# Performance work log

Measured on AMD Instinct MI355X. Metric: run time of the kernel, lower is better.

## Reference

```python
import jax, jax.numpy as jnp
import numpy as np

V, EMB, HID, ENC = 32000, 512, 1024, 1024
B, T, TB = 64, 512, 512
PAD = 0


def setup_inputs() -> dict:
    key = jax.random.key(0)
    kk = jax.random.split(key, 24)
    w = lambda k, s: jax.random.normal(k, s, dtype=jnp.float32) * 0.02
    a = lambda k, s: jax.random.normal(k, s, dtype=jnp.float32)
    emb_table = w(kk[0], (V, EMB)).at[PAD].set(0.0)  # padding_idx row zeroed
    IN = EMB + ENC + HID  # lstm input size
    return {
        "y": jax.random.randint(kk[1], (B,), 0, V),
        "h": a(kk[2], (B, HID)),
        "c": a(kk[3], (B, HID)),
        "enc_out": a(kk[4], (B, T, ENC)),
        "bwd_states": a(kk[5], (B, TB, HID)),
        "src_ids": jax.random.randint(kk[6], (B, T), 0, V),
        "src_mask": jnp.ones((B, T), dtype=jnp.int32),
        "emb_table": emb_table,
        "W_ih": w(kk[7], (4 * HID, IN)),
        "W_hh": w(kk[8], (4 * HID, HID)),
        "b_ih": jnp.zeros((4 * HID,), jnp.float32),
        "b_hh": jnp.zeros((4 * HID,), jnp.float32),
        "Wq_e": w(kk[9], (HID, HID)),
        "Wk_e": w(kk[10], (HID, ENC)),
        "v_e": w(kk[11], (HID,)),
        "Wq_b": w(kk[12], (HID, HID)),
        "Wk_b": w(kk[13], (HID, HID)),
        "v_b": w(kk[14], (HID,)),
        "Wp": w(kk[15], (V, HID)),
        "bp": jnp.zeros((V,), jnp.float32),
        "wc": w(kk[16], (ENC,)),
        "ws": w(kk[17], (HID,)),
        "wy": w(kk[18], (EMB,)),
        "pg_b": jnp.zeros((), jnp.float32),
    }


def _bahdanau(query, keys, Wq, Wk, v, mask=None):
    # query [B,H], keys [B,T,D] -> context [B,D], attn [B,T]
    q = query @ Wq.T                                  # [B,A]
    k = jnp.einsum("btd,ad->bta", keys, Wk)           # [B,T,A]
    e = jnp.einsum("bta,a->bt", jnp.tanh(q[:, None, :] + k), v)
    if mask is not None:
        e = jnp.where(mask == 0, jnp.finfo(e.dtype).min, e)
    attn = jax.nn.softmax(e, axis=-1)
    ctx = jnp.einsum("bt,btd->bd", attn, keys)
    return ctx, attn


def reference(y, h, c, enc_out, bwd_states, src_ids, src_mask, emb_table,
              W_ih, W_hh, b_ih, b_hh, Wq_e, Wk_e, v_e, Wq_b, Wk_b, v_b,
              Wp, bp, wc, ws, wy, pg_b):
    emb = emb_table[y]                                # [B,EMB]
    query = h                                         # state[0].squeeze(0)
    c_enc, attn_enc = _bahdanau(query, enc_out, Wq_e, Wk_e, v_e, src_mask)
    c_bwd, _ = _bahdanau(query, bwd_states, Wq_b, Wk_b, v_b)
    x = jnp.concatenate([emb, c_enc, c_bwd], axis=-1)  # [B,EMB+ENC+HID]
    gates = x @ W_ih.T + h @ W_hh.T + b_ih + b_hh      # [B,4H], torch order i,f,g,o
    i, f, g, o = jnp.split(gates, 4, axis=-1)
    c_new = jax.nn.sigmoid(f) * c + jax.nn.sigmoid(i) * jnp.tanh(g)
    h_new = jax.nn.sigmoid(o) * jnp.tanh(c_new)
    vocab_dist = jax.nn.softmax(h_new @ Wp.T + bp, axis=-1)  # [B,V]
    p_gen = jax.nn.sigmoid(c_enc @ wc + h_new @ ws + emb @ wy + pg_b)[:, None]
    p_vocab = p_gen * vocab_dist
    copy_mask = (src_ids < V).astype(vocab_dist.dtype)
    safe_ids = jnp.minimum(src_ids, V - 1)
    contrib = (1.0 - p_gen) * attn_enc * copy_mask     # [B,T]
    scatter = jax.vmap(lambda idx, val: jnp.zeros((V,), val.dtype).at[idx].add(val))(safe_ids, contrib)
    final_dist = p_vocab + scatter
    return final_dist, h_new, c_new
```

## Files before the change

kernel.cpp:

```cpp
#include <hip/hip_runtime.h>
#include <hip/hip_bf16.h>

#define VSZ   32000
#define EMBD  512
#define HIDD  1024
#define BB    64
#define TSEQ  512
#define G4    4096

typedef short bf16x8 __attribute__((ext_vector_type(8)));
typedef float f32x4  __attribute__((ext_vector_type(4)));
typedef float f32x16 __attribute__((ext_vector_type(16)));

__device__ __forceinline__ float sigmoid_f(float x){ return 1.0f/(1.0f+__expf(-x)); }
__device__ __forceinline__ float fast_tanh(float x){
  float e = __expf(2.0f*x);
  return 1.0f - 2.0f*__builtin_amdgcn_rcpf(e + 1.0f);
}
__device__ __forceinline__ short f2bfs(float x){
  unsigned u = __float_as_uint(x);
  unsigned r = (u + 0x7FFFu + ((u>>16)&1u)) >> 16;
  return (short)r;
}
__device__ __forceinline__ bf16x8 cvt8(float4 a, float4 b){
  bf16x8 p;
  p[0]=f2bfs(a.x); p[1]=f2bfs(a.y); p[2]=f2bfs(a.z); p[3]=f2bfs(a.w);
  p[4]=f2bfs(b.x); p[5]=f2bfs(b.y); p[6]=f2bfs(b.z); p[7]=f2bfs(b.w);
  return p;
}
__device__ __forceinline__ float wave_sum(float x){
  #pragma unroll
  for (int off=32; off>0; off>>=1) x += __shfl_xor(x, off);
  return x;
}
__device__ __forceinline__ float wave_max(float x){
  #pragma unroll
  for (int off=32; off>0; off>>=1) x = fmaxf(x, __shfl_xor(x, off));
  return x;
}

__global__ __launch_bounds__(128) void k_embed(const int* __restrict__ y,
                                               const float* __restrict__ tab,
                                               float* __restrict__ emb){
  int b = blockIdx.x;
  int row = y[b];
  const float4* src = (const float4*)(tab + (size_t)row*EMBD);
  float4* dst = (float4*)(emb + (size_t)b*EMBD);
  dst[threadIdx.x] = src[threadIdx.x];
}

__global__ __launch_bounds__(256) void k_pack(const float* __restrict__ Wk,
                                              short* __restrict__ dst){
  int id = blockIdx.x*256 + threadIdx.x;
  int l = id & 63, s = (id>>6) & 63, nt = id >> 12;
  const float* src = Wk + (size_t)(nt*32 + (l&31))*1024 + s*16 + (l>>5)*8;
  float4 f0 = ((const float4*)src)[0], f1 = ((const float4*)src)[1];
  *(bf16x8*)(dst + (size_t)id*8) = cvt8(f0, f1);
}

__global__ __launch_bounds__(256) void k_prep_h(const float* __restrict__ h,
                                                short* __restrict__ xb){
  int id = blockIdx.x*256 + threadIdx.x;
  int b = id >> 7, d = (id & 127)*8;
  const float4* s = (const float4*)(h + (size_t)b*HIDD + d);
  *(bf16x8*)(xb + (size_t)b*3584 + 2560 + d) = cvt8(s[0], s[1]);
}

__global__ __launch_bounds__(256) void k_prep_x2(const float* __restrict__ emb,
                                                 const float* __restrict__ ctxe,
                                                 const float* __restrict__ ctxb,
                                                 short* __restrict__ xb){
  int id = blockIdx.x*256 + threadIdx.x;
  if (id >= 64*320) return;
  int b = id / 320, off = (id % 320)*8;
  const float* src;
  if (off < 512)        src = emb  + (size_t)b*EMBD + off;
  else if (off < 1536)  src = ctxe + (size_t)b*HIDD + (off-512);
  else                  src = ctxb + (size_t)b*HIDD + (off-1536);
  float4 f0 = ((const float4*)src)[0], f1 = ((const float4*)src)[1];
  *(bf16x8*)(xb + (size_t)b*3584 + off) = cvt8(f0, f1);
}

__global__ __launch_bounds__(256) void k_mm64(
    const short* __restrict__ A0, int lda0, const float* __restrict__ B0, int ldb0, int K0, float* __restrict__ out0, int ldo0,
    const short* __restrict__ A1, int lda1, const float* __restrict__ B1, int ldb1, int K1, float* __restrict__ out1, int ldo1){
  const short* A; const float* B; float* out; int lda, ldb, K, ldo;
  if (blockIdx.z == 0){ A=A0; B=B0; out=out0; lda=lda0; ldb=ldb0; K=K0; ldo=ldo0; }
  else                { A=A1; B=B1; out=out1; lda=lda1; ldb=ldb1; K=K1; ldo=ldo1; }
  int tid = threadIdx.x, l = tid & 63, w = tid >> 6;
  int l15 = l & 15, l4 = l >> 4;
  int n0 = blockIdx.x*256 + w*64;
  int kper = K / gridDim.y;
  int dbeg = blockIdx.y * kper, dend = dbeg + kper;
  f32x4 acc[4][4];
  #pragma unroll
  for (int i=0;i<4;i++)
    #pragma unroll
    for (int j=0;j<4;j++)
      #pragma unroll
      for (int r=0;r<4;r++) acc[i][j][r]=0.f;
  for (int d0=dbeg; d0<dend; d0+=32){
    bf16x8 af[4];
    #pragma unroll
    for (int ms=0; ms<4; ms++)
      af[ms] = *(const bf16x8*)(A + (size_t)(ms*16 + l15)*lda + d0 + l4*8);
    bf16x8 bfr[4];
    #pragma unroll
    for (int ni=0; ni<4; ni++){
      const float* bp = B + (size_t)(n0 + ni*16 + l15)*ldb + d0 + l4*8;
      float4 f0 = ((const float4*)bp)[0], f1 = ((const float4*)bp)[1];
      bfr[ni] = cvt8(f0, f1);
    }
    #pragma unroll
    for (int ms=0; ms<4; ms++)
      #pragma unroll
      for (int ni=0; ni<4; ni++)
        acc[ms][ni] = __builtin_amdgcn_mfma_f32_16x16x32_bf16(af[ms], bfr[ni], acc[ms][ni], 0,0,0);
  }
  float* op = out + (size_t)blockIdx.y * 64 * ldo;
  #pragma unroll
  for (int ms=0; ms<4; ms++)
    #pragma unroll
    for (int ni=0; ni<4; ni++)
      #pragma unroll
      for (int r=0; r<4; r++){
        int m = ms*16 + l4*4 + r;
        op[(size_t)m*ldo + n0 + ni*16 + l15] = acc[ms][ni][r];
      }
}

__global__ __launch_bounds__(256) void k_qred(const float* __restrict__ qpe,
                                              const float* __restrict__ qpb,
                                              float* __restrict__ qe,
                                              float* __restrict__ qb){
  int id = blockIdx.x*256 + threadIdx.x;
  int sel = id >> 16, i = id & 65535;
  const float* p = (sel ? qpb : qpe) + i;
  (sel ? qb : qe)[i] = p[0] + p[65536];
}

__global__ __launch_bounds__(512,2) void k_energy(
    const float* __restrict__ enc, const float* __restrict__ bwd,
    const short* __restrict__ pke, const short* __restrict__ pkb,
    const float* __restrict__ qe_, const float* __restrict__ qb_,
    const float* __restrict__ ve, const float* __restrict__ vb,
    const int* __restrict__ mask,
    float* __restrict__ out_e, float* __restrict__ out_b){
  __shared__ short A_s[2][64*128];
  __shared__ float ebuf[8][64];
  int att = blockIdx.z;
  const float* keys = att ? bwd : enc;
  const short* pk   = att ? pkb : pke;
  const float* q    = att ? qb_ : qe_;
  const float* v    = att ? vb  : ve;
  int b = blockIdx.y, t0 = blockIdx.x*64;
  int tid = threadIdx.x;
  int l = tid & 63, w = tid >> 6;
  int lhi = l >> 5, l31 = l & 31;

  int sr = tid >> 3, sf = tid & 7;
  const float4* ssrc = (const float4*)(keys + ((size_t)(b*TSEQ + t0 + sr))*1024 + sf*16);
  char* swb0 = (char*)A_s + sr*256 + ((sf*32)      ^ ((sr&7)<<4));
  char* swb1 = (char*)A_s + sr*256 + ((sf*32 + 16) ^ ((sr&7)<<4));

  const bf16x8* Bp = ((const bf16x8*)pk) + (size_t)(w*4)*64*64 + l;
  int rb0 = l31*256, rb1 = (l31+32)*256;
  int xorv = (l31&7)<<4;

  f32x16 acc0[4], acc1[4];
  #pragma unroll
  for (int at=0; at<4; at++)
    #pragma unroll
    for (int r=0;r<16;r++){ acc0[at][r]=0.f; acc1[at][r]=0.f; }

  float4 st[4];
  st[0]=ssrc[0]; st[1]=ssrc[1]; st[2]=ssrc[2]; st[3]=ssrc[3];
  *(bf16x8*)(swb0) = cvt8(st[0], st[1]);
  *(bf16x8*)(swb1) = cvt8(st[2], st[3]);
  __syncthreads();
  st[0]=ssrc[32]; st[1]=ssrc[33]; st[2]=ssrc[34]; st[3]=ssrc[35];

  for (int c=0; c<8; ++c){
    const char* base = (const char*)A_s + (c&1)*16384;
    #pragma unroll
    for (int ss=0; ss<8; ++ss){
      int s = c*8 + ss;
      int off = ((ss*32 + lhi*16) ^ xorv);
      bf16x8 a0 = *(const bf16x8*)(base + rb0 + off);
      bf16x8 a1 = *(const bf16x8*)(base + rb1 + off);
      bf16x8 b0 = Bp[(0*64+s)*64];
      bf16x8 b1 = Bp[(1*64+s)*64];
      bf16x8 b2 = Bp[(2*64+s)*64];
      bf16x8 b3 = Bp[(3*64+s)*64];
      acc0[0] = __builtin_amdgcn_mfma_f32_32x32x16_bf16(a0, b0, acc0[0], 0,0,0);
      acc1[0] = __builtin_amdgcn_mfma_f32_32x32x16_bf16(a1, b0, acc1[0], 0,0,0);
      acc0[1] = __builtin_amdgcn_mfma_f32_32x32x16_bf16(a0, b1, acc0[1], 0,0,0);
      acc1[1] = __builtin_amdgcn_mfma_f32_32x32x16_bf16(a1, b1, acc1[1], 0,0,0);
      acc0[2] = __builtin_amdgcn_mfma_f32_32x32x16_bf16(a0, b2, acc0[2], 0,0,0);
      acc1[2] = __builtin_amdgcn_mfma_f32_32x32x16_bf16(a1, b2, acc1[2], 0,0,0);
      acc0[3] = __builtin_amdgcn_mfma_f32_32x32x16_bf16(a0, b3, acc0[3], 0,0,0);
      acc1[3] = __builtin_amdgcn_mfma_f32_32x32x16_bf16(a1, b3, acc1[3], 0,0,0);
    }
    if (c < 7){
      char* dst = (char*)A_s + ((c+1)&1)*16384;
      *(bf16x8*)(dst + (swb0 - (char*)A_s)) = cvt8(st[0], st[1]);
      *(bf16x8*)(dst + (swb1 - (char*)A_s)) = cvt8(st[2], st[3]);
      if (c < 6){
        const float4* s4 = ssrc + (c+2)*32;
        st[0]=s4[0]; st[1]=s4[1]; st[2]=s4[2]; st[3]=s4[3];
      }
    }
    __syncthreads();
  }

  float ep0[16], ep1[16];
  #pragma unroll
  for (int r=0;r<16;r++){ ep0[r]=0.f; ep1[r]=0.f; }
  #pragma unroll
  for (int at=0; at<4; at++){
    int a = w*128 + at*32 + l31;
    float qv = q[(size_t)b*HIDD + a];
    float vv = v[a];
    #pragma unroll
    for (int r=0;r<16;r++){
      ep0[r] += vv * fast_tanh(qv + acc0[at][r]);
      ep1[r] += vv * fast_tanh(qv + acc1[at][r]);
    }
  }
  #pragma unroll
  for (int r=0;r<16;r++){
    float x = ep0[r];
    x += __shfl_xor(x,1); x += __shfl_xor(x,2); x += __shfl_xor(x,4);
    x += __shfl_xor(x,8); x += __shfl_xor(x,16);
    ep0[r] = x;
    float y = ep1[r];
    y += __shfl_xor(y,1); y += __shfl_xor(y,2); y += __shfl_xor(y,4);
    y += __shfl_xor(y,8); y += __shfl_xor(y,16);
    ep1[r] = y;
  }
  if (l31 == 0){
    #pragma unroll
    for (int r=0;r<16;r++){
      int t = (r&3) + 8*(r>>2) + 4*lhi;
      ebuf[w][t]      = ep0[r];
      ebuf[w][t + 32] = ep1[r];
    }
  }
  __syncthreads();
  if (tid < 64){
    float s = 0.f;
    #pragma unroll
    for (int ww=0; ww<8; ww++) s += ebuf[ww][tid];
    int t = t0 + tid;
    if (att==0 && mask[(size_t)b*TSEQ + t]==0) s = -3.4e38f;
    (att ? out_b : out_e)[(size_t)b*TSEQ + t] = s;
  }
}

__global__ __launch_bounds__(256) void k_softmax_t(float* __restrict__ e_enc,
                                                   float* __restrict__ e_bwd){
  float* e = (blockIdx.y==0 ? e_enc : e_bwd) + (size_t)blockIdx.x*TSEQ;
  __shared__ float red[8];
  int tid = threadIdx.x, lane = tid & 63, w = tid >> 6;
  float v0 = e[tid], v1 = e[tid+256];
  float m = wave_max(fmaxf(v0, v1));
  if (lane==0) red[w] = m;
  __syncthreads();
  m = fmaxf(fmaxf(red[0],red[1]), fmaxf(red[2],red[3]));
  float x0 = __expf(v0-m), x1 = __expf(v1-m);
  float s = wave_sum(x0+x1);
  if (lane==0) red[4+w] = s;
  __syncthreads();
  s = red[4]+red[5]+red[6]+red[7];
  float inv = 1.0f/s;
  e[tid] = x0*inv; e[tid+256] = x1*inv;
}

__global__ __launch_bounds__(256) void k_ctx(const float* __restrict__ enc,
                                             const float* __restrict__ bwdst,
                                             const float* __restrict__ att_e,
                                             const float* __restrict__ att_b,
                                             float* __restrict__ ctxp){
  int b = blockIdx.x, sel = blockIdx.y, s = blockIdx.z;
  const float* keys = (sel ? bwdst : enc) + ((size_t)b*TSEQ + s*64)*1024;
  const float* att  = (sel ? att_b : att_e) + (size_t)b*TSEQ + s*64;
  int tid = threadIdx.x;
  float acc[4] = {0.f,0.f,0.f,0.f};
  for (int t=0;t<64;t++){
    float a = att[t];
    #pragma unroll
    for (int i=0;i<4;i++) acc[i] += a*keys[(size_t)t*1024 + i*256 + tid];
  }
  float* o = ctxp + (((size_t)sel*BB + b)*8 + s)*1024;
  #pragma unroll
  for (int i=0;i<4;i++) o[i*256+tid] = acc[i];
}

__global__ __launch_bounds__(256) void k_ctxred(const float* __restrict__ ctxp,
                                                float* __restrict__ ctx_e,
                                                float* __restrict__ ctx_b){
  int id = blockIdx.x*256 + threadIdx.x;
  int sel = id >> 16; int rem = id & 65535; int b = rem >> 10; int d = rem & 1023;
  const float* p = ctxp + (((size_t)sel*BB + b)*8)*1024 + d;
  float s = 0.f;
  #pragma unroll
  for (int i=0;i<8;i++) s += p[i*1024];
  (sel ? ctx_b : ctx_e)[(size_t)b*HIDD + d] = s;
}

__global__ __launch_bounds__(256) void k_lstm(const float* __restrict__ gp,
                                              const float* __restrict__ b_ih,
                                              const float* __restrict__ b_hh,
                                              const float* __restrict__ c_old,
                                              float* __restrict__ out,
                                              short* __restrict__ hb){
  int id = blockIdx.x*256 + threadIdx.x;
  int b = id >> 10, j = id & 1023;
  size_t base = (size_t)b*G4;
  float gs[4];
  #pragma unroll
  for (int g=0; g<4; g++){
    int col = g*1024 + j;
    float s = b_ih[col] + b_hh[col];
    #pragma unroll
    for (int k=0;k<8;k++) s += gp[(size_t)k*(64*G4) + base + col];
    gs[g] = s;
  }
  float ig = sigmoid_f(gs[0]);
  float fg = sigmoid_f(gs[1]);
  float gg = tanhf(gs[2]);
  float og = sigmoid_f(gs[3]);
  float cn = fg*c_old[id] + ig*gg;
  float hn = og*tanhf(cn);
  out[(size_t)BB*VSZ + id] = hn;
  out[(size_t)BB*VSZ + (size_t)BB*HIDD + id] = cn;
  hb[id] = f2bfs(hn);
}

__global__ __launch_bounds__(256) void k_vocab2(const short* __restrict__ hb,
                                                const float* __restrict__ Wp,
                                                const float* __restrict__ bp,
                                                float* __restrict__ out){
  int tid = threadIdx.x, l = tid & 63, w = tid >> 6;
  int l15 = l & 15, l4 = l >> 4;
  int n0 = blockIdx.x*256 + w*64;
  f32x4 acc[4][4];
  #pragma unroll
  for (int i=0;i<4;i++)
    #pragma unroll
    for (int j=0;j<4;j++)
      #pragma unroll
      for (int r=0;r<4;r++) acc[i][j][r]=0.f;
  for (int d0=0; d0<1024; d0+=32){
    bf16x8 af[4];
    #pragma unroll
    for (int ms=0; ms<4; ms++)
      af[ms] = *(const bf16x8*)(hb + (size_t)(ms*16 + l15)*1024 + d0 + l4*8);
    bf16x8 bfr[4];
    #pragma unroll
    for (int ni=0; ni<4; ni++){
      const float* bpp = Wp + (size_t)(n0 + ni*16 + l15)*1024 + d0 + l4*8;
      float4 f0 = ((const float4*)bpp)[0], f1 = ((const float4*)bpp)[1];
      bfr[ni] = cvt8(f0, f1);
    }
    #pragma unroll
    for (int ms=0; ms<4; ms++)
      #pragma unroll
      for (int ni=0; ni<4; ni++)
        acc[ms][ni] = __builtin_amdgcn_mfma_f32_16x16x32_bf16(af[ms], bfr[ni], acc[ms][ni], 0,0,0);
  }
  #pragma unroll
  for (int ms=0; ms<4; ms++)
    #pragma unroll
    for (int ni=0; ni<4; ni++)
      #pragma unroll
      for (int r=0; r<4; r++){
        int m = ms*16 + l4*4 + r;
        int n = n0 + ni*16 + l15;
        out[(size_t)m*VSZ + n] = acc[ms][ni][r] + bp[n];
      }
}

__global__ __launch_bounds__(1024) void k_final(const float* __restrict__ ctxe,
                                                const float* __restrict__ emb,
                                                const float* __restrict__ wc,
                                                const float* __restrict__ wsv,
                                                const float* __restrict__ wy,
                                                const float* __restrict__ pgb,
                                                float* __restrict__ out,
                                                float* __restrict__ pgen_ws){
  __shared__ float red[32];
  int b = blockIdx.x, tid = threadIdx.x, lane = tid & 63, w = tid >> 6;
  const float* hn = out + (size_t)BB*VSZ + (size_t)b*HIDD;
  float acc = ctxe[(size_t)b*HIDD + tid]*wc[tid] + hn[tid]*wsv[tid];
  if (tid < 512) acc += emb[(size_t)b*EMBD + tid]*wy[tid];
  acc = wave_sum(acc);
  if (lane==0) red[w] = acc;
  __syncthreads();
  float s0 = pgb[0];
  #pragma unroll
  for (int i=0;i<16;i++) s0 += red[i];
  float pg = sigmoid_f(s0);
  if (tid==0) pgen_ws[b] = pg;
  __syncthreads();

  float* row = out + (size_t)b*VSZ;
  float m = -3.4e38f;
  for (int i=tid;i<VSZ;i+=1024) m = fmaxf(m, row[i]);
  m = wave_max(m);
  if (lane==0) red[w] = m;
  __syncthreads();
  #pragma unroll
  for (int i=0;i<16;i++) m = fmaxf(m, red[i]);
  float s = 0.f;
  for (int i=tid;i<VSZ;i+=1024) s += __expf(row[i]-m);
  s = wave_sum(s);
  if (lane==0) red[16+w] = s;
  __syncthreads();
  float tot = 0.f;
  #pragma unroll
  for (int i=0;i<16;i++) tot += red[16+i];
  float scale = pg / tot;
  for (int i=tid;i<VSZ;i+=1024) row[i] = __expf(row[i]-m)*scale;
}

__global__ __launch_bounds__(256) void k_scatter(const int* __restrict__ src_ids,
                                                 const float* __restrict__ att_e,
                                                 const float* __restrict__ pgen_ws,
                                                 float* __restrict__ out){
  int id = blockIdx.x*256 + threadIdx.x;
  int b = id >> 9;
  float pg = pgen_ws[b];
  int sid = src_ids[id];
  float contrib = (1.0f - pg) * att_e[id] * (sid < VSZ ? 1.0f : 0.0f);
  int safe = sid < VSZ-1 ? sid : VSZ-1;
  atomicAdd(&out[(size_t)b*VSZ + safe], contrib);
}

extern "C" void kernel_launch(void* const* d_in, const int* in_sizes, int n_in,
                              void* d_out, int out_size, void* d_ws, size_t ws_size,
                              hipStream_t stream){
  const int*   y     = (const int*)d_in[0];
  const float* h     = (const float*)d_in[1];
  const float* c     = (const float*)d_in[2];
  const float* enc   = (const float*)d_in[3];
  const float* bwd   = (const float*)d_in[4];
  const int*   sids  = (const int*)d_in[5];
  const int*   smask = (const int*)d_in[6];
  const float* tab   = (const float*)d_in[7];
  const float* W_ih  = (const float*)d_in[8];
  const float* W_hh  = (const float*)d_in[9];
  const float* b_ih  = (const float*)d_in[10];
  const float* b_hh  = (const float*)d_in[11];
  const float* Wq_e  = (const float*)d_in[12];
  const float* Wk_e  = (const float*)d_in[13];
  const float* v_e   = (const float*)d_in[14];
  const float* Wq_b  = (const float*)d_in[15];
  const float* Wk_b  = (const float*)d_in[16];
  const float* v_b   = (const float*)d_in[17];
  const float* Wp    = (const float*)d_in[18];
  const float* bp    = (const float*)d_in[19];
  const float* wc    = (const float*)d_in[20];
  const float* wsv   = (const float*)d_in[21];
  const float* wy    = (const float*)d_in[22];
  const float* pgb   = (const float*)d_in[23];
  float* out = (float*)d_out;

  float* W = (float*)d_ws;
  float* ws_emb  = W; W += BB*EMBD;
  float* ws_qe   = W; W += BB*HIDD;
  float* ws_qb   = W; W += BB*HIDD;
  float* ws_atte = W; W += BB*TSEQ;
  float* ws_attb = W; W += BB*TSEQ;
  float* ws_ctxe = W; W += BB*HIDD;
  float* ws_ctxb = W; W += BB*HIDD;
  float* ws_ctxp = W; W += 2*BB*8*1024;
  float* ws_pgen = W; W += 64;
  float* ws_qpe  = W; W += 2*BB*HIDD;
  float* ws_qpb  = W; W += 2*BB*HIDD;
  float* ws_gp   = W; W += 8*BB*G4;
  short* xb      = (short*)W; W += (BB*3584)/2;
  short* hb      = (short*)W; W += (BB*HIDD)/2;
  short* pk_e    = (short*)W; W += (HIDD*HIDD)/2;
  short* pk_b    = (short*)W; W += (HIDD*HIDD)/2;

  k_embed<<<BB, 128, 0, stream>>>(y, tab, ws_emb);
  k_pack<<<512, 256, 0, stream>>>(Wk_e, pk_e);
  k_pack<<<512, 256, 0, stream>>>(Wk_b, pk_b);
  k_prep_h<<<32, 256, 0, stream>>>(h, xb);
  k_mm64<<<dim3(4,2,2), 256, 0, stream>>>(
      xb+2560, 3584, Wq_e, 1024, 1024, ws_qpe, 1024,
      xb+2560, 3584, Wq_b, 1024, 1024, ws_qpb, 1024);
  k_qred<<<512, 256, 0, stream>>>(ws_qpe, ws_qpb, ws_qe, ws_qb);
  k_energy<<<dim3(8,BB,2), 512, 0, stream>>>(enc, bwd, pk_e, pk_b,
      ws_qe, ws_qb, v_e, v_b, smask, ws_atte, ws_attb);
  k_softmax_t<<<dim3(BB,2), 256, 0, stream>>>(ws_atte, ws_attb);
  k_ctx<<<dim3(BB,2,8), 256, 0, stream>>>(enc, bwd, ws_atte, ws_attb, ws_ctxp);
  k_ctxred<<<512, 256, 0, stream>>>(ws_ctxp, ws_ctxe, ws_ctxb);
  k_prep_x2<<<80, 256, 0, stream>>>(ws_emb, ws_ctxe, ws_ctxb, xb);
  k_mm64<<<dim3(16,4,2), 256, 0, stream>>>(
      xb,      3584, W_ih, 2560, 2560, ws_gp,             G4,
      xb+2560, 3584, W_hh, 1024, 1024, ws_gp + 4*BB*G4,   G4);
  k_lstm<<<256, 256, 0, stream>>>(ws_gp, b_ih, b_hh, c, out, hb);
  k_vocab2<<<125, 256, 0, stream>>>(hb, Wp, bp, out);
  k_final<<<BB, 1024, 0, stream>>>(ws_ctxe, ws_emb, wc, wsv, wy, pgb, out, ws_pgen);
  k_scatter<<<128, 256, 0, stream>>>(sids, ws_atte, ws_pgen, out);
}
```

Before: 436.8 us.

## Split energy kernel by attention half, fold small kernels, widen vocab grid

The energy kernel now runs 256-thread blocks, each covering half of the attention dimension. Launches become 32x64, and the partial energies are written to a buffer that the softmax kernel sums and masks. The q split-K reduction is folded into the energy epilogue, and the embedding gather is folded into prep_x2 and k_final, so two small launches disappear. The vocab GEMM now uses 128-column blocks with 250 blocks to spread work across more CUs, which means each Wp tile is converted to bf16 twice. The aim is fewer launches and higher occupancy, at the cost of extra partial-sum traffic and redundant Wp reads.

```diff
diff --git a/kernel.cpp b/kernel.cpp
--- a/kernel.cpp
+++ b/kernel.cpp
@@ -39,16 +39,6 @@
   return x;
 }
 
-__global__ __launch_bounds__(128) void k_embed(const int* __restrict__ y,
-                                               const float* __restrict__ tab,
-                                               float* __restrict__ emb){
-  int b = blockIdx.x;
-  int row = y[b];
-  const float4* src = (const float4*)(tab + (size_t)row*EMBD);
-  float4* dst = (float4*)(emb + (size_t)b*EMBD);
-  dst[threadIdx.x] = src[threadIdx.x];
-}
-
 __global__ __launch_bounds__(256) void k_pack(const float* __restrict__ Wk,
                                               short* __restrict__ dst){
   int id = blockIdx.x*256 + threadIdx.x;
@@ -66,7 +56,8 @@
   *(bf16x8*)(xb + (size_t)b*3584 + 2560 + d) = cvt8(s[0], s[1]);
 }
 
-__global__ __launch_bounds__(256) void k_prep_x2(const float* __restrict__ emb,
+__global__ __launch_bounds__(256) void k_prep_x2(const float* __restrict__ tab,
+                                                 const int* __restrict__ y,
                                                  const float* __restrict__ ctxe,
                                                  const float* __restrict__ ctxb,
                                                  short* __restrict__ xb){
@@ -74,7 +65,7 @@
   if (id >= 64*320) return;
   int b = id / 320, off = (id % 320)*8;
   const float* src;
-  if (off < 512)        src = emb  + (size_t)b*EMBD + off;
+  if (off < 512)        src = tab  + (size_t)y[b]*EMBD + off;
   else if (off < 1536)  src = ctxe + (size_t)b*HIDD + (off-512);
   else                  src = ctxb + (size_t)b*HIDD + (off-1536);
   float4 f0 = ((const float4*)src)[0], f1 = ((const float4*)src)[1];
@@ -129,43 +120,34 @@
       }
 }
 
-__global__ __launch_bounds__(256) void k_qred(const float* __restrict__ qpe,
-                                              const float* __restrict__ qpb,
-                                              float* __restrict__ qe,
-                                              float* __restrict__ qb){
-  int id = blockIdx.x*256 + threadIdx.x;
-  int sel = id >> 16, i = id & 65535;
-  const float* p = (sel ? qpb : qpe) + i;
-  (sel ? qb : qe)[i] = p[0] + p[65536];
-}
-
-__global__ __launch_bounds__(512,2) void k_energy(
+__global__ __launch_bounds__(256,2) void k_energy(
     const float* __restrict__ enc, const float* __restrict__ bwd,
     const short* __restrict__ pke, const short* __restrict__ pkb,
-    const float* __restrict__ qe_, const float* __restrict__ qb_,
+    const float* __restrict__ qpe, const float* __restrict__ qpb,
     const float* __restrict__ ve, const float* __restrict__ vb,
-    const int* __restrict__ mask,
-    float* __restrict__ out_e, float* __restrict__ out_b){
+    float* __restrict__ ep_out){
   __shared__ short A_s[2][64*128];
-  __shared__ float ebuf[8][64];
-  int att = blockIdx.z;
+  __shared__ float ebuf[4][64];
+  int bx = blockIdx.x;
+  int half = bx & 1, att = (bx>>1) & 1, t0 = (bx>>2)*64;
   const float* keys = att ? bwd : enc;
   const short* pk   = att ? pkb : pke;
-  const float* q    = att ? qb_ : qe_;
+  const float* qp   = att ? qpb : qpe;
   const float* v    = att ? vb  : ve;
-  int b = blockIdx.y, t0 = blockIdx.x*64;
-  int tid = threadIdx.x;
-  int l = tid & 63, w = tid >> 6;
+  int b = blockIdx.y;
+  int tid = threadIdx.x, l = tid & 63, w = tid >> 6;
   int lhi = l >> 5, l31 = l & 31;
 
-  int sr = tid >> 3, sf = tid & 7;
-  const float4* ssrc = (const float4*)(keys + ((size_t)(b*TSEQ + t0 + sr))*1024 + sf*16);
-  char* swb0 = (char*)A_s + sr*256 + ((sf*32)      ^ ((sr&7)<<4));
-  char* swb1 = (char*)A_s + sr*256 + ((sf*32 + 16) ^ ((sr&7)<<4));
-
-  const bf16x8* Bp = ((const bf16x8*)pk) + (size_t)(w*4)*64*64 + l;
+  int sr = tid >> 2, sf = tid & 3;
+  const float4* ssrc = (const float4*)(keys + ((size_t)(b*TSEQ + t0 + sr))*1024) + sf*8;
+  char* swb = (char*)A_s + sr*256;
+  int wsw[4];
+  #pragma unroll
+  for (int j=0;j<4;j++) wsw[j] = (((sf*4+j)<<4) ^ ((sr&15)<<4));
+
+  const bf16x8* Bp = ((const bf16x8*)pk) + ((size_t)(half*16 + w*4)*64)*64 + l;
   int rb0 = l31*256, rb1 = (l31+32)*256;
-  int xorv = (l31&7)<<4;
+  int xorv = (l31&15)<<4;
 
   f32x16 acc0[4], acc1[4];
   #pragma unroll
@@ -173,25 +155,27 @@
     #pragma unroll
     for (int r=0;r<16;r++){ acc0[at][r]=0.f; acc1[at][r]=0.f; }
 
-  float4 st[4];
-  st[0]=ssrc[0]; st[1]=ssrc[1]; st[2]=ssrc[2]; st[3]=ssrc[3];
-  *(bf16x8*)(swb0) = cvt8(st[0], st[1]);
-  *(bf16x8*)(swb1) = cvt8(st[2], st[3]);
-  __syncthreads();
-  st[0]=ssrc[32]; st[1]=ssrc[33]; st[2]=ssrc[34]; st[3]=ssrc[35];
+  float4 st[8];
+  #pragma unroll
+  for (int i=0;i<8;i++) st[i] = ssrc[i];
+  #pragma unroll
+  for (int j=0;j<4;j++) *(bf16x8*)(swb + wsw[j]) = cvt8(st[2*j], st[2*j+1]);
+  __syncthreads();
+  #pragma unroll
+  for (int i=0;i<8;i++) st[i] = ssrc[32 + i];
 
   for (int c=0; c<8; ++c){
     const char* base = (const char*)A_s + (c&1)*16384;
     #pragma unroll
     for (int ss=0; ss<8; ++ss){
       int s = c*8 + ss;
-      int off = ((ss*32 + lhi*16) ^ xorv);
-      bf16x8 a0 = *(const bf16x8*)(base + rb0 + off);
-      bf16x8 a1 = *(const bf16x8*)(base + rb1 + off);
       bf16x8 b0 = Bp[(0*64+s)*64];
       bf16x8 b1 = Bp[(1*64+s)*64];
       bf16x8 b2 = Bp[(2*64+s)*64];
       bf16x8 b3 = Bp[(3*64+s)*64];
+      int off = (((ss*2 + lhi)<<4) ^ xorv);
+      bf16x8 a0 = *(const bf16x8*)(base + rb0 + off);
+      bf16x8 a1 = *(const bf16x8*)(base + rb1 + off);
       acc0[0] = __builtin_amdgcn_mfma_f32_32x32x16_bf16(a0, b0, acc0[0], 0,0,0);
       acc1[0] = __builtin_amdgcn_mfma_f32_32x32x16_bf16(a1, b0, acc1[0], 0,0,0);
       acc0[1] = __builtin_amdgcn_mfma_f32_32x32x16_bf16(a0, b1, acc0[1], 0,0,0);
@@ -202,12 +186,12 @@
       acc1[3] = __builtin_amdgcn_mfma_f32_32x32x16_bf16(a1, b3, acc1[3], 0,0,0);
     }
     if (c < 7){
-      char* dst = (char*)A_s + ((c+1)&1)*16384;
-      *(bf16x8*)(dst + (swb0 - (char*)A_s)) = cvt8(st[0], st[1]);
-      *(bf16x8*)(dst + (swb1 - (char*)A_s)) = cvt8(st[2], st[3]);
+      char* dst = (char*)A_s + ((c+1)&1)*16384 + sr*256;
+      #pragma unroll
+      for (int j=0;j<4;j++) *(bf16x8*)(dst + wsw[j]) = cvt8(st[2*j], st[2*j+1]);
       if (c < 6){
-        const float4* s4 = ssrc + (c+2)*32;
-        st[0]=s4[0]; st[1]=s4[1]; st[2]=s4[2]; st[3]=s4[3];
+        #pragma unroll
+        for (int i=0;i<8;i++) st[i] = ssrc[(c+2)*32 + i];
       }
     }
     __syncthreads();
@@ -218,8 +202,8 @@
   for (int r=0;r<16;r++){ ep0[r]=0.f; ep1[r]=0.f; }
   #pragma unroll
   for (int at=0; at<4; at++){
-    int a = w*128 + at*32 + l31;
-    float qv = q[(size_t)b*HIDD + a];
+    int a = half*512 + w*128 + at*32 + l31;
+    float qv = qp[(size_t)b*HIDD + a] + qp[65536 + (size_t)b*HIDD + a];
     float vv = v[a];
     #pragma unroll
     for (int r=0;r<16;r++){
@@ -250,19 +234,27 @@
   if (tid < 64){
     float s = 0.f;
     #pragma unroll
-    for (int ww=0; ww<8; ww++) s += ebuf[ww][tid];
-    int t = t0 + tid;
-    if (att==0 && mask[(size_t)b*TSEQ + t]==0) s = -3.4e38f;
-    (att ? out_b : out_e)[(size_t)b*TSEQ + t] = s;
-  }
-}
-
-__global__ __launch_bounds__(256) void k_softmax_t(float* __restrict__ e_enc,
-                                                   float* __restrict__ e_bwd){
-  float* e = (blockIdx.y==0 ? e_enc : e_bwd) + (size_t)blockIdx.x*TSEQ;
+    for (int ww=0; ww<4; ww++) s += ebuf[ww][tid];
+    ep_out[(((size_t)att*2 + half)*BB + b)*TSEQ + t0 + tid] = s;
+  }
+}
+
+__global__ __launch_bounds__(256) void k_softmax_t(const float* __restrict__ ep,
+                                                   const int* __restrict__ mask,
+                                                   float* __restrict__ att_e,
+                                                   float* __restrict__ att_b){
+  int b = blockIdx.x, att = blockIdx.y;
+  const float* p0 = ep + (((size_t)att*2 + 0)*BB + b)*TSEQ;
+  const float* p1 = ep + (((size_t)att*2 + 1)*BB + b)*TSEQ;
+  float* e = (att ? att_b : att_e) + (size_t)b*TSEQ;
   __shared__ float red[8];
   int tid = threadIdx.x, lane = tid & 63, w = tid >> 6;
-  float v0 = e[tid], v1 = e[tid+256];
+  float v0 = p0[tid] + p1[tid];
+  float v1 = p0[tid+256] + p1[tid+256];
+  if (att==0){
+    if (mask[(size_t)b*TSEQ + tid]==0)      v0 = -3.4e38f;
+    if (mask[(size_t)b*TSEQ + tid+256]==0)  v1 = -3.4e38f;
+  }
   float m = wave_max(fmaxf(v0, v1));
   if (lane==0) red[w] = m;
   __syncthreads();
@@ -343,19 +335,20 @@
                                                 float* __restrict__ out){
   int tid = threadIdx.x, l = tid & 63, w = tid >> 6;
   int l15 = l & 15, l4 = l >> 4;
-  int n0 = blockIdx.x*256 + w*64;
-  f32x4 acc[4][4];
-  #pragma unroll
-  for (int i=0;i<4;i++)
+  int mh = w >> 1;
+  int n0 = blockIdx.x*128 + (w&1)*64;
+  f32x4 acc[2][4];
+  #pragma unroll
+  for (int i=0;i<2;i++)
     #pragma unroll
     for (int j=0;j<4;j++)
       #pragma unroll
       for (int r=0;r<4;r++) acc[i][j][r]=0.f;
   for (int d0=0; d0<1024; d0+=32){
-    bf16x8 af[4];
-    #pragma unroll
-    for (int ms=0; ms<4; ms++)
-      af[ms] = *(const bf16x8*)(hb + (size_t)(ms*16 + l15)*1024 + d0 + l4*8);
+    bf16x8 af[2];
+    #pragma unroll
+    for (int ms=0; ms<2; ms++)
+      af[ms] = *(const bf16x8*)(hb + (size_t)(mh*32 + ms*16 + l15)*1024 + d0 + l4*8);
     bf16x8 bfr[4];
     #pragma unroll
     for (int ni=0; ni<4; ni++){
@@ -364,25 +357,26 @@
       bfr[ni] = cvt8(f0, f1);
     }
     #pragma unroll
-    for (int ms=0; ms<4; ms++)
+    for (int ms=0; ms<2; ms++)
       #pragma unroll
       for (int ni=0; ni<4; ni++)
         acc[ms][ni] = __builtin_amdgcn_mfma_f32_16x16x32_bf16(af[ms], bfr[ni], acc[ms][ni], 0,0,0);
   }
   #pragma unroll
-  for (int ms=0; ms<4; ms++)
+  for (int ms=0; ms<2; ms++)
     #pragma unroll
     for (int ni=0; ni<4; ni++)
       #pragma unroll
       for (int r=0; r<4; r++){
-        int m = ms*16 + l4*4 + r;
+        int m = mh*32 + ms*16 + l4*4 + r;
         int n = n0 + ni*16 + l15;
         out[(size_t)m*VSZ + n] = acc[ms][ni][r] + bp[n];
       }
 }
 
 __global__ __launch_bounds__(1024) void k_final(const float* __restrict__ ctxe,
-                                                const float* __restrict__ emb,
+                                                const float* __restrict__ tab,
+                                                const int* __restrict__ y,
                                                 const float* __restrict__ wc,
                                                 const float* __restrict__ wsv,
                                                 const float* __restrict__ wy,
@@ -393,7 +387,7 @@
   int b = blockIdx.x, tid = threadIdx.x, lane = tid & 63, w = tid >> 6;
   const float* hn = out + (size_t)BB*VSZ + (size_t)b*HIDD;
   float acc = ctxe[(size_t)b*HIDD + tid]*wc[tid] + hn[tid]*wsv[tid];
-  if (tid < 512) acc += emb[(size_t)b*EMBD + tid]*wy[tid];
+  if (tid < 512) acc += tab[(size_t)y[b]*EMBD + tid]*wy[tid];
   acc = wave_sum(acc);
   if (lane==0) red[w] = acc;
   __syncthreads();
@@ -467,42 +461,38 @@
   float* out = (float*)d_out;
 
   float* W = (float*)d_ws;
-  float* ws_emb  = W; W += BB*EMBD;
-  float* ws_qe   = W; W += BB*HIDD;
-  float* ws_qb   = W; W += BB*HIDD;
+  float* ws_qpe  = W; W += 2*BB*HIDD;
+  float* ws_qpb  = W; W += 2*BB*HIDD;
+  float* ws_ep   = W; W += 4*BB*TSEQ;
   float* ws_atte = W; W += BB*TSEQ;
   float* ws_attb = W; W += BB*TSEQ;
   float* ws_ctxe = W; W += BB*HIDD;
   float* ws_ctxb = W; W += BB*HIDD;
   float* ws_ctxp = W; W += 2*BB*8*1024;
   float* ws_pgen = W; W += 64;
-  float* ws_qpe  = W; W += 2*BB*HIDD;
-  float* ws_qpb  = W; W += 2*BB*HIDD;
   float* ws_gp   = W; W += 8*BB*G4;
   short* xb      = (short*)W; W += (BB*3584)/2;
   short* hb      = (short*)W; W += (BB*HIDD)/2;
   short* pk_e    = (short*)W; W += (HIDD*HIDD)/2;
   short* pk_b    = (short*)W; W += (HIDD*HIDD)/2;
 
-  k_embed<<<BB, 128, 0, stream>>>(y, tab, ws_emb);
   k_pack<<<512, 256, 0, stream>>>(Wk_e, pk_e);
   k_pack<<<512, 256, 0, stream>>>(Wk_b, pk_b);
   k_prep_h<<<32, 256, 0, stream>>>(h, xb);
   k_mm64<<<dim3(4,2,2), 256, 0, stream>>>(
       xb+2560, 3584, Wq_e, 1024, 1024, ws_qpe, 1024,
       xb+2560, 3584, Wq_b, 1024, 1024, ws_qpb, 1024);
-  k_qred<<<512, 256, 0, stream>>>(ws_qpe, ws_qpb, ws_qe, ws_qb);
-  k_energy<<<dim3(8,BB,2), 512, 0, stream>>>(enc, bwd, pk_e, pk_b,
-      ws_qe, ws_qb, v_e, v_b, smask, ws_atte, ws_attb);
-  k_softmax_t<<<dim3(BB,2), 256, 0, stream>>>(ws_atte, ws_attb);
+  k_energy<<<dim3(32,BB), 256, 0, stream>>>(enc, bwd, pk_e, pk_b,
+      ws_qpe, ws_qpb, v_e, v_b, ws_ep);
+  k_softmax_t<<<dim3(BB,2), 256, 0, stream>>>(ws_ep, smask, ws_atte, ws_attb);
   k_ctx<<<dim3(BB,2,8), 256, 0, stream>>>(enc, bwd, ws_atte, ws_attb, ws_ctxp);
   k_ctxred<<<512, 256, 0, stream>>>(ws_ctxp, ws_ctxe, ws_ctxb);
-  k_prep_x2<<<80, 256, 0, stream>>>(ws_emb, ws_ctxe, ws_ctxb, xb);
+  k_prep_x2<<<80, 256, 0, stream>>>(tab, y, ws_ctxe, ws_ctxb, xb);
   k_mm64<<<dim3(16,4,2), 256, 0, stream>>>(
       xb,      3584, W_ih, 2560, 2560, ws_gp,             G4,
       xb+2560, 3584, W_hh, 1024, 1024, ws_gp + 4*BB*G4,   G4);
   k_lstm<<<256, 256, 0, stream>>>(ws_gp, b_ih, b_hh, c, out, hb);
-  k_vocab2<<<125, 256, 0, stream>>>(hb, Wp, bp, out);
-  k_final<<<BB, 1024, 0, stream>>>(ws_ctxe, ws_emb, wc, wsv, wy, pgb, out, ws_pgen);
+  k_vocab2<<<250, 256, 0, stream>>>(hb, Wp, bp, out);
+  k_final<<<BB, 1024, 0, stream>>>(ws_ctxe, tab, y, wc, wsv, wy, pgb, out, ws_pgen);
   k_scatter<<<128, 256, 0, stream>>>(sids, ws_atte, ws_pgen, out);
 }
```

New measurement: 432.9 us. No clear change (-0.9%).

## Fuse embed and qred kernels, prefetch B fragments, use hardware bf16 convert, split vocab grid

Applied to the files above, without the earlier changes.

Removes the separate embedding-gather and q-partial-reduction kernels by reading the table row directly in consumers and summing the two split-K partials inside the energy kernel. Replaces software bf16 rounding with the packed v_cvt_pk_bf16_f32 instruction. Software-pipelines the packed-key B loads one step ahead in the energy MFMA loop. Splits the vocab projection so each block covers 128 columns with waves split over M, doubling block count to 250 for better CU coverage, at the cost of each Wp tile being loaded and converted twice.

```diff
diff --git a/kernel.cpp b/kernel.cpp
--- a/kernel.cpp
+++ b/kernel.cpp
@@ -22,11 +22,16 @@
   unsigned r = (u + 0x7FFFu + ((u>>16)&1u)) >> 16;
   return (short)r;
 }
+__device__ __forceinline__ unsigned cvtpk(float a, float b){
+  unsigned r;
+  asm("v_cvt_pk_bf16_f32 %0, %1, %2" : "=v"(r) : "v"(a), "v"(b));
+  return r;
+}
 __device__ __forceinline__ bf16x8 cvt8(float4 a, float4 b){
-  bf16x8 p;
-  p[0]=f2bfs(a.x); p[1]=f2bfs(a.y); p[2]=f2bfs(a.z); p[3]=f2bfs(a.w);
-  p[4]=f2bfs(b.x); p[5]=f2bfs(b.y); p[6]=f2bfs(b.z); p[7]=f2bfs(b.w);
-  return p;
+  union { unsigned u[4]; bf16x8 v; } o;
+  o.u[0]=cvtpk(a.x,a.y); o.u[1]=cvtpk(a.z,a.w);
+  o.u[2]=cvtpk(b.x,b.y); o.u[3]=cvtpk(b.z,b.w);
+  return o.v;
 }
 __device__ __forceinline__ float wave_sum(float x){
   #pragma unroll
@@ -37,16 +42,6 @@
   #pragma unroll
   for (int off=32; off>0; off>>=1) x = fmaxf(x, __shfl_xor(x, off));
   return x;
-}
-
-__global__ __launch_bounds__(128) void k_embed(const int* __restrict__ y,
-                                               const float* __restrict__ tab,
-                                               float* __restrict__ emb){
-  int b = blockIdx.x;
-  int row = y[b];
-  const float4* src = (const float4*)(tab + (size_t)row*EMBD);
-  float4* dst = (float4*)(emb + (size_t)b*EMBD);
-  dst[threadIdx.x] = src[threadIdx.x];
 }
 
 __global__ __launch_bounds__(256) void k_pack(const float* __restrict__ Wk,
@@ -66,7 +61,8 @@
   *(bf16x8*)(xb + (size_t)b*3584 + 2560 + d) = cvt8(s[0], s[1]);
 }
 
-__global__ __launch_bounds__(256) void k_prep_x2(const float* __restrict__ emb,
+__global__ __launch_bounds__(256) void k_prep_x2(const float* __restrict__ tab,
+                                                 const int* __restrict__ y,
                                                  const float* __restrict__ ctxe,
                                                  const float* __restrict__ ctxb,
                                                  short* __restrict__ xb){
@@ -74,7 +70,7 @@
   if (id >= 64*320) return;
   int b = id / 320, off = (id % 320)*8;
   const float* src;
-  if (off < 512)        src = emb  + (size_t)b*EMBD + off;
+  if (off < 512)        src = tab  + (size_t)y[b]*EMBD + off;
   else if (off < 1536)  src = ctxe + (size_t)b*HIDD + (off-512);
   else                  src = ctxb + (size_t)b*HIDD + (off-1536);
   float4 f0 = ((const float4*)src)[0], f1 = ((const float4*)src)[1];
@@ -129,20 +125,10 @@
       }
 }
 
-__global__ __launch_bounds__(256) void k_qred(const float* __restrict__ qpe,
-                                              const float* __restrict__ qpb,
-                                              float* __restrict__ qe,
-                                              float* __restrict__ qb){
-  int id = blockIdx.x*256 + threadIdx.x;
-  int sel = id >> 16, i = id & 65535;
-  const float* p = (sel ? qpb : qpe) + i;
-  (sel ? qb : qe)[i] = p[0] + p[65536];
-}
-
 __global__ __launch_bounds__(512,2) void k_energy(
     const float* __restrict__ enc, const float* __restrict__ bwd,
     const short* __restrict__ pke, const short* __restrict__ pkb,
-    const float* __restrict__ qe_, const float* __restrict__ qb_,
+    const float* __restrict__ qpe, const float* __restrict__ qpb,
     const float* __restrict__ ve, const float* __restrict__ vb,
     const int* __restrict__ mask,
     float* __restrict__ out_e, float* __restrict__ out_b){
@@ -151,7 +137,7 @@
   int att = blockIdx.z;
   const float* keys = att ? bwd : enc;
   const short* pk   = att ? pkb : pke;
-  const float* q    = att ? qb_ : qe_;
+  const float* qp   = att ? qpb : qpe;
   const float* v    = att ? vb  : ve;
   int b = blockIdx.y, t0 = blockIdx.x*64;
   int tid = threadIdx.x;
@@ -165,7 +151,7 @@
 
   const bf16x8* Bp = ((const bf16x8*)pk) + (size_t)(w*4)*64*64 + l;
   int rb0 = l31*256, rb1 = (l31+32)*256;
-  int xorv = (l31&7)<<4;
+  int xorv = (l31&7)<<4, boff = lhi*16;
 
   f32x16 acc0[4], acc1[4];
   #pragma unroll
@@ -180,18 +166,25 @@
   __syncthreads();
   st[0]=ssrc[32]; st[1]=ssrc[33]; st[2]=ssrc[34]; st[3]=ssrc[35];
 
+  bf16x8 bn0 = Bp[0*64];
+  bf16x8 bn1 = Bp[64*64];
+  bf16x8 bn2 = Bp[128*64];
+  bf16x8 bn3 = Bp[192*64];
+
   for (int c=0; c<8; ++c){
     const char* base = (const char*)A_s + (c&1)*16384;
     #pragma unroll
     for (int ss=0; ss<8; ++ss){
       int s = c*8 + ss;
-      int off = ((ss*32 + lhi*16) ^ xorv);
+      bf16x8 b0 = bn0, b1 = bn1, b2 = bn2, b3 = bn3;
+      int sp1 = (s < 63) ? s+1 : 63;
+      bn0 = Bp[(  0 + sp1)*64];
+      bn1 = Bp[( 64 + sp1)*64];
+      bn2 = Bp[(128 + sp1)*64];
+      bn3 = Bp[(192 + sp1)*64];
+      int off = ((ss*32 + boff) ^ xorv);
       bf16x8 a0 = *(const bf16x8*)(base + rb0 + off);
       bf16x8 a1 = *(const bf16x8*)(base + rb1 + off);
-      bf16x8 b0 = Bp[(0*64+s)*64];
-      bf16x8 b1 = Bp[(1*64+s)*64];
-      bf16x8 b2 = Bp[(2*64+s)*64];
-      bf16x8 b3 = Bp[(3*64+s)*64];
       acc0[0] = __builtin_amdgcn_mfma_f32_32x32x16_bf16(a0, b0, acc0[0], 0,0,0);
       acc1[0] = __builtin_amdgcn_mfma_f32_32x32x16_bf16(a1, b0, acc1[0], 0,0,0);
       acc0[1] = __builtin_amdgcn_mfma_f32_32x32x16_bf16(a0, b1, acc0[1], 0,0,0);
@@ -219,7 +212,7 @@
   #pragma unroll
   for (int at=0; at<4; at++){
     int a = w*128 + at*32 + l31;
-    float qv = q[(size_t)b*HIDD + a];
+    float qv = qp[(size_t)b*HIDD + a] + qp[65536 + (size_t)b*HIDD + a];
     float vv = v[a];
     #pragma unroll
     for (int r=0;r<16;r++){
@@ -343,19 +336,20 @@
                                                 float* __restrict__ out){
   int tid = threadIdx.x, l = tid & 63, w = tid >> 6;
   int l15 = l & 15, l4 = l >> 4;
-  int n0 = blockIdx.x*256 + w*64;
-  f32x4 acc[4][4];
-  #pragma unroll
-  for (int i=0;i<4;i++)
+  int mh = w >> 1;
+  int n0 = blockIdx.x*128 + (w&1)*64;
+  f32x4 acc[2][4];
+  #pragma unroll
+  for (int i=0;i<2;i++)
     #pragma unroll
     for (int j=0;j<4;j++)
       #pragma unroll
       for (int r=0;r<4;r++) acc[i][j][r]=0.f;
   for (int d0=0; d0<1024; d0+=32){
-    bf16x8 af[4];
-    #pragma unroll
-    for (int ms=0; ms<4; ms++)
-      af[ms] = *(const bf16x8*)(hb + (size_t)(ms*16 + l15)*1024 + d0 + l4*8);
+    bf16x8 af[2];
+    #pragma unroll
+    for (int ms=0; ms<2; ms++)
+      af[ms] = *(const bf16x8*)(hb + (size_t)(mh*32 + ms*16 + l15)*1024 + d0 + l4*8);
     bf16x8 bfr[4];
     #pragma unroll
     for (int ni=0; ni<4; ni++){
@@ -364,25 +358,26 @@
       bfr[ni] = cvt8(f0, f1);
     }
     #pragma unroll
-    for (int ms=0; ms<4; ms++)
+    for (int ms=0; ms<2; ms++)
       #pragma unroll
       for (int ni=0; ni<4; ni++)
         acc[ms][ni] = __builtin_amdgcn_mfma_f32_16x16x32_bf16(af[ms], bfr[ni], acc[ms][ni], 0,0,0);
   }
   #pragma unroll
-  for (int ms=0; ms<4; ms++)
+  for (int ms=0; ms<2; ms++)
     #pragma unroll
     for (int ni=0; ni<4; ni++)
       #pragma unroll
       for (int r=0; r<4; r++){
-        int m = ms*16 + l4*4 + r;
+        int m = mh*32 + ms*16 + l4*4 + r;
         int n = n0 + ni*16 + l15;
         out[(size_t)m*VSZ + n] = acc[ms][ni][r] + bp[n];
       }
 }
 
 __global__ __launch_bounds__(1024) void k_final(const float* __restrict__ ctxe,
-                                                const float* __restrict__ emb,
+                                                const float* __restrict__ tab,
+                                                const int* __restrict__ y,
                                                 const float* __restrict__ wc,
                                                 const float* __restrict__ wsv,
                                                 const float* __restrict__ wy,
@@ -393,7 +388,7 @@
   int b = blockIdx.x, tid = threadIdx.x, lane = tid & 63, w = tid >> 6;
   const float* hn = out + (size_t)BB*VSZ + (size_t)b*HIDD;
   float acc = ctxe[(size_t)b*HIDD + tid]*wc[tid] + hn[tid]*wsv[tid];
-  if (tid < 512) acc += emb[(size_t)b*EMBD + tid]*wy[tid];
+  if (tid < 512) acc += tab[(size_t)y[b]*EMBD + tid]*wy[tid];
   acc = wave_sum(acc);
   if (lane==0) red[w] = acc;
   __syncthreads();
@@ -467,42 +462,37 @@
   float* out = (float*)d_out;
 
   float* W = (float*)d_ws;
-  float* ws_emb  = W; W += BB*EMBD;
-  float* ws_qe   = W; W += BB*HIDD;
-  float* ws_qb   = W; W += BB*HIDD;
+  float* ws_qpe  = W; W += 2*BB*HIDD;
+  float* ws_qpb  = W; W += 2*BB*HIDD;
   float* ws_atte = W; W += BB*TSEQ;
   float* ws_attb = W; W += BB*TSEQ;
   float* ws_ctxe = W; W += BB*HIDD;
   float* ws_ctxb = W; W += BB*HIDD;
   float* ws_ctxp = W; W += 2*BB*8*1024;
   float* ws_pgen = W; W += 64;
-  float* ws_qpe  = W; W += 2*BB*HIDD;
-  float* ws_qpb  = W; W += 2*BB*HIDD;
   float* ws_gp   = W; W += 8*BB*G4;
   short* xb      = (short*)W; W += (BB*3584)/2;
   short* hb      = (short*)W; W += (BB*HIDD)/2;
   short* pk_e    = (short*)W; W += (HIDD*HIDD)/2;
   short* pk_b    = (short*)W; W += (HIDD*HIDD)/2;
 
-  k_embed<<<BB, 128, 0, stream>>>(y, tab, ws_emb);
   k_pack<<<512, 256, 0, stream>>>(Wk_e, pk_e);
   k_pack<<<512, 256, 0, stream>>>(Wk_b, pk_b);
   k_prep_h<<<32, 256, 0, stream>>>(h, xb);
   k_mm64<<<dim3(4,2,2), 256, 0, stream>>>(
       xb+2560, 3584, Wq_e, 1024, 1024, ws_qpe, 1024,
       xb+2560, 3584, Wq_b, 1024, 1024, ws_qpb, 1024);
-  k_qred<<<512, 256, 0, stream>>>(ws_qpe, ws_qpb, ws_qe, ws_qb);
   k_energy<<<dim3(8,BB,2), 512, 0, stream>>>(enc, bwd, pk_e, pk_b,
-      ws_qe, ws_qb, v_e, v_b, smask, ws_atte, ws_attb);
+      ws_qpe, ws_qpb, v_e, v_b, smask, ws_atte, ws_attb);
   k_softmax_t<<<dim3(BB,2), 256, 0, stream>>>(ws_atte, ws_attb);
   k_ctx<<<dim3(BB,2,8), 256, 0, stream>>>(enc, bwd, ws_atte, ws_attb, ws_ctxp);
   k_ctxred<<<512, 256, 0, stream>>>(ws_ctxp, ws_ctxe, ws_ctxb);
-  k_prep_x2<<<80, 256, 0, stream>>>(ws_emb, ws_ctxe, ws_ctxb, xb);
+  k_prep_x2<<<80, 256, 0, stream>>>(tab, y, ws_ctxe, ws_ctxb, xb);
   k_mm64<<<dim3(16,4,2), 256, 0, stream>>>(
       xb,      3584, W_ih, 2560, 2560, ws_gp,             G4,
       xb+2560, 3584, W_hh, 1024, 1024, ws_gp + 4*BB*G4,   G4);
   k_lstm<<<256, 256, 0, stream>>>(ws_gp, b_ih, b_hh, c, out, hb);
-  k_vocab2<<<125, 256, 0, stream>>>(hb, Wp, bp, out);
-  k_final<<<BB, 1024, 0, stream>>>(ws_ctxe, ws_emb, wc, wsv, wy, pgb, out, ws_pgen);
+  k_vocab2<<<250, 256, 0, stream>>>(hb, Wp, bp, out);
+  k_final<<<BB, 1024, 0, stream>>>(ws_ctxe, tab, y, wc, wsv, wy, pgb, out, ws_pgen);
   k_scatter<<<128, 256, 0, stream>>>(sids, ws_atte, ws_pgen, out);
 }
```

New measurement: 400.2 us. 1.09x faster.
